# Performance work log

Hardware: AMD Instinct MI355X
Metric: run time of the kernel (lower is better)

The kernel has to match this reference:

```python
import jax, jax.numpy as jnp
import numpy as np

TOKENS, D_IN, D_OUT, RANK = 16384, 4096, 4096, 512

def setup_inputs() -> dict:
    key = jax.random.key(0)
    k1, k2, k3, k4 = jax.random.split(key, 4)
    x = jax.random.normal(k1, (TOKENS, D_IN), dtype=jnp.float32)
    U = jax.random.normal(k2, (D_OUT, RANK), dtype=jnp.float32) * 0.02
    sigma = jax.random.uniform(k3, (RANK,), dtype=jnp.float32)
    V = jax.random.normal(k4, (D_IN, RANK), dtype=jnp.float32) * 0.02
    return {"x": x, "U": U, "sigma": sigma, "V": V}

def reference(x, U, sigma, V):
    # W = U @ diag(sigma) @ V.T  (shape [out, in]); out = x @ W.T
    # diag(sigma) contraction expressed as a column scale of U (same math).
    W = (U * sigma[None, :]) @ V.T          # [out, in]
    return x @ W.T                          # [tokens, out]
```

## Files before the change

kernel.cpp:

```cpp
#include <hip/hip_runtime.h>

typedef __bf16 bf16;
typedef __bf16 bf16x4 __attribute__((ext_vector_type(4)));
typedef __bf16 bf16x8 __attribute__((ext_vector_type(8)));
typedef float  f32x4  __attribute__((ext_vector_type(4)));

#define TOKENS 16384
#define D_IN   4096
#define D_OUT  4096
#define RANK   512

__device__ inline void gload_lds16(const bf16* g, bf16* l) {
    __builtin_amdgcn_global_load_lds((const __attribute__((address_space(1))) void*)g,
                                     (__attribute__((address_space(3))) void*)l,
                                     16, 0, 0);
}

__global__ __launch_bounds__(256) void vt_scale(const float* __restrict__ V,
                                                const float* __restrict__ sg,
                                                bf16* __restrict__ Vst) {
    __shared__ float tile[64][65];
    const int tx = threadIdx.x & 63;
    const int ty = threadIdx.x >> 6;
    const int kb = blockIdx.x * 64;
    const int rb = blockIdx.y * 64;
    const float s = sg[rb + tx];
#pragma unroll
    for (int i = ty; i < 64; i += 4)
        tile[i][tx] = V[(size_t)(kb + i) * RANK + rb + tx] * s;
    __syncthreads();
#pragma unroll
    for (int i = ty; i < 64; i += 4) {
        int r = rb + i;
        int kp = kb + (tx ^ ((r & 7) << 3));
        Vst[(size_t)r * D_IN + kp] = (bf16)tile[tx][i];
    }
}

__global__ __launch_bounds__(256) void cvt_bf16_4(const float* __restrict__ in,
                                                  bf16* __restrict__ o, int n4) {
    int i = blockIdx.x * 256 + threadIdx.x;
    if (i < n4) {
        f32x4 v = *(const f32x4*)(in + (size_t)i * 4);
        bf16x4 b = { (bf16)v[0], (bf16)v[1], (bf16)v[2], (bf16)v[3] };
        *(bf16x4*)(o + (size_t)i * 4) = b;
    }
}

__global__ __launch_bounds__(256) void gemm1_swz(const float* __restrict__ A,
                                                 const bf16* __restrict__ B,
                                                 bf16* __restrict__ T,
                                                 int M, int N, int K) {
    __shared__ bf16 Al[128 * 64];
    __shared__ bf16 Bl[128 * 64];

    const int t  = threadIdx.x;
    const int l  = t & 63;
    const int w  = t >> 6;
    const int wr = w >> 1, wc = w & 1;
    const int lr = l & 15;
    const int kg = l >> 4;
    const int sxor = (lr & 7) << 3;

    const int nwg = gridDim.x;
    const int bid = blockIdx.x;
    const int cpx = nwg >> 3;
    const int swz = (bid & 7) * cpx + (bid >> 3);
    const int ntn = N >> 7;
    const int tm  = (swz / ntn) << 7;
    const int tn  = (swz % ntn) << 7;

    const int arow  = t >> 4;
    const int acg   = t & 15;
    const int awxor = (arow & 7) << 3;
    const float* Ap = A + (size_t)(tm + arow) * K + acg * 4;
    const bf16* Bp  = B + (size_t)(tn + (t >> 3)) * K + (t & 7) * 8;

    f32x4 acc[4][4] = {};

    for (int kt = 0; kt < K; kt += 64) {
#pragma unroll
        for (int c = 0; c < 4; ++c)
            gload_lds16(Bp + kt + (size_t)(c * 32) * K, &Bl[(c * 256 + t) * 8]);
        f32x4 ra[8];
#pragma unroll
        for (int c = 0; c < 8; ++c)
            ra[c] = *(const f32x4*)(Ap + kt + (size_t)(c * 16) * K);
#pragma unroll
        for (int c = 0; c < 8; ++c) {
            bf16x4 b = { (bf16)ra[c][0], (bf16)ra[c][1], (bf16)ra[c][2], (bf16)ra[c][3] };
            *(bf16x4*)&Al[(c * 16 + arow) * 64 + ((acg * 4) ^ awxor)] = b;
        }
        __syncthreads();

#pragma unroll
        for (int ks = 0; ks < 2; ++ks) {
            bf16x8 af[4], bfr[4];
#pragma unroll
            for (int f = 0; f < 4; ++f) {
                af[f]  = *(const bf16x8*)&Al[(wr * 64 + f * 16 + lr) * 64 + ((ks * 32 + kg * 8) ^ sxor)];
                bfr[f] = *(const bf16x8*)&Bl[(wc * 64 + f * 16 + lr) * 64 + ((ks * 32 + kg * 8) ^ sxor)];
            }
#pragma unroll
            for (int fm = 0; fm < 4; ++fm)
#pragma unroll
                for (int fn = 0; fn < 4; ++fn)
                    acc[fm][fn] = __builtin_amdgcn_mfma_f32_16x16x32_bf16(
                        af[fm], bfr[fn], acc[fm][fn], 0, 0, 0);
        }
        __syncthreads();
    }

    const int r0 = tm + wr * 64 + kg * 4;
    const int c0 = tn + wc * 64 + lr;
#pragma unroll
    for (int fm = 0; fm < 4; ++fm)
#pragma unroll
        for (int fn = 0; fn < 4; ++fn)
#pragma unroll
            for (int r = 0; r < 4; ++r)
                T[(size_t)(r0 + fm * 16 + r) * N + (c0 + fn * 16)] = (bf16)acc[fm][fn][r];
}

__global__ __launch_bounds__(256) void gemm2_bt(const bf16* __restrict__ A,
                                                const bf16* __restrict__ B,
                                                float* __restrict__ out,
                                                int M, int N, int K) {
    __shared__ bf16 Al[128 * 64];
    __shared__ bf16 Bl[128 * 64];

    const int t  = threadIdx.x;
    const int l  = t & 63;
    const int w  = t >> 6;
    const int wr = w >> 1, wc = w & 1;
    const int lr = l & 15;
    const int kg = l >> 4;

    const int nwg = gridDim.x;
    const int bid = blockIdx.x;
    const int cpx = nwg >> 3;
    const int swz = (bid & 7) * cpx + (bid >> 3);
    const int ntn = N >> 7;
    const int tm  = (swz / ntn) << 7;
    const int tn  = (swz % ntn) << 7;

    f32x4 acc[4][4] = {};

    for (int kt = 0; kt < K; kt += 64) {
#pragma unroll
        for (int c = 0; c < 4; ++c) {
            int i = c * 256 + t;
            gload_lds16(A + (size_t)(tm + (i >> 3)) * K + kt + (i & 7) * 8, &Al[i * 8]);
        }
#pragma unroll
        for (int c = 0; c < 4; ++c) {
            int i = c * 256 + t;
            gload_lds16(B + (size_t)(tn + (i >> 3)) * K + kt + (i & 7) * 8, &Bl[i * 8]);
        }
        __syncthreads();

#pragma unroll
        for (int ks = 0; ks < 2; ++ks) {
            bf16x8 af[4], bfr[4];
#pragma unroll
            for (int f = 0; f < 4; ++f) {
                af[f]  = *(const bf16x8*)&Al[(wr * 64 + f * 16 + lr) * 64 + ks * 32 + kg * 8];
                bfr[f] = *(const bf16x8*)&Bl[(wc * 64 + f * 16 + lr) * 64 + ks * 32 + kg * 8];
            }
#pragma unroll
            for (int fm = 0; fm < 4; ++fm)
#pragma unroll
                for (int fn = 0; fn < 4; ++fn)
                    acc[fm][fn] = __builtin_amdgcn_mfma_f32_16x16x32_bf16(
                        af[fm], bfr[fn], acc[fm][fn], 0, 0, 0);
        }
        __syncthreads();
    }

    const int r0 = tm + wr * 64 + kg * 4;
    const int c0 = tn + wc * 64 + lr;
#pragma unroll
    for (int fm = 0; fm < 4; ++fm)
#pragma unroll
        for (int fn = 0; fn < 4; ++fn)
#pragma unroll
            for (int r = 0; r < 4; ++r)
                out[(size_t)(r0 + fm * 16 + r) * N + (c0 + fn * 16)] = acc[fm][fn][r];
}

extern "C" void kernel_launch(void* const* d_in, const int* in_sizes, int n_in,
                              void* d_out, int out_size, void* d_ws, size_t ws_size,
                              hipStream_t stream) {
    const float* x  = (const float*)d_in[0];
    const float* U  = (const float*)d_in[1];
    const float* sg = (const float*)d_in[2];
    const float* V  = (const float*)d_in[3];
    float* out = (float*)d_out;

    char* ws = (char*)d_ws;
    bf16* Vst = (bf16*)ws;
    bf16* Ub  = (bf16*)(ws + (4u << 20));
    bf16* T   = (bf16*)(ws + (8u << 20));

    vt_scale<<<dim3(D_IN / 64, RANK / 64), 256, 0, stream>>>(V, sg, Vst);
    cvt_bf16_4<<<(D_OUT * RANK / 4 + 255) / 256, 256, 0, stream>>>(U, Ub, D_OUT * RANK / 4);

    gemm1_swz<<<(TOKENS / 128) * (RANK / 128), 256, 0, stream>>>(
        x, Vst, T, TOKENS, RANK, D_IN);

    gemm2_bt<<<(TOKENS / 128) * (D_OUT / 128), 256, 0, stream>>>(
        T, Ub, out, TOKENS, D_OUT, RANK);
}
```

Before: 268.3 us.

## Split-K the first GEMM into two halves with a separate reduction kernel

The first GEMM (x @ Vs^T) originally launched only 512 workgroups, each looping over the full K=4096. It now launches 1024 workgroups, each handling half of K, and writes fp32 partial sums to a workspace. A new reduce kernel adds the two partials and converts the sum to bf16 T. The intent is more workgroups in flight on the many-CU GPU, at the cost of an extra kernel launch and about 64 MB of extra fp32 traffic for the partials.

```diff
diff --git a/kernel.cpp b/kernel.cpp
--- a/kernel.cpp
+++ b/kernel.cpp
@@ -47,10 +47,10 @@
     }
 }
 
-__global__ __launch_bounds__(256) void gemm1_swz(const float* __restrict__ A,
-                                                 const bf16* __restrict__ B,
-                                                 bf16* __restrict__ T,
-                                                 int M, int N, int K) {
+__global__ __launch_bounds__(256) void gemm1_sk(const float* __restrict__ A,
+                                                const bf16* __restrict__ B,
+                                                float* __restrict__ P,
+                                                int M, int N, int Kfull, int Khalf) {
     __shared__ bf16 Al[128 * 64];
     __shared__ bf16 Bl[128 * 64];
 
@@ -66,26 +66,29 @@
     const int bid = blockIdx.x;
     const int cpx = nwg >> 3;
     const int swz = (bid & 7) * cpx + (bid >> 3);
+    const int khalf  = swz >> 9;
+    const int tileid = swz & 511;
     const int ntn = N >> 7;
-    const int tm  = (swz / ntn) << 7;
-    const int tn  = (swz % ntn) << 7;
+    const int tm  = (tileid / ntn) << 7;
+    const int tn  = (tileid % ntn) << 7;
+    const int kbase = khalf * Khalf;
 
     const int arow  = t >> 4;
     const int acg   = t & 15;
     const int awxor = (arow & 7) << 3;
-    const float* Ap = A + (size_t)(tm + arow) * K + acg * 4;
-    const bf16* Bp  = B + (size_t)(tn + (t >> 3)) * K + (t & 7) * 8;
+    const float* Ap = A + (size_t)(tm + arow) * Kfull + kbase + acg * 4;
+    const bf16* Bp  = B + (size_t)(tn + (t >> 3)) * Kfull + kbase + (t & 7) * 8;
 
     f32x4 acc[4][4] = {};
 
-    for (int kt = 0; kt < K; kt += 64) {
+    for (int kt = 0; kt < Khalf; kt += 64) {
 #pragma unroll
         for (int c = 0; c < 4; ++c)
-            gload_lds16(Bp + kt + (size_t)(c * 32) * K, &Bl[(c * 256 + t) * 8]);
+            gload_lds16(Bp + kt + (size_t)(c * 32) * Kfull, &Bl[(c * 256 + t) * 8]);
         f32x4 ra[8];
 #pragma unroll
         for (int c = 0; c < 8; ++c)
-            ra[c] = *(const f32x4*)(Ap + kt + (size_t)(c * 16) * K);
+            ra[c] = *(const f32x4*)(Ap + kt + (size_t)(c * 16) * Kfull);
 #pragma unroll
         for (int c = 0; c < 8; ++c) {
             bf16x4 b = { (bf16)ra[c][0], (bf16)ra[c][1], (bf16)ra[c][2], (bf16)ra[c][3] };
@@ -111,6 +114,7 @@
         __syncthreads();
     }
 
+    float* Po = P + (size_t)khalf * M * N;
     const int r0 = tm + wr * 64 + kg * 4;
     const int c0 = tn + wc * 64 + lr;
 #pragma unroll
@@ -119,7 +123,20 @@
         for (int fn = 0; fn < 4; ++fn)
 #pragma unroll
             for (int r = 0; r < 4; ++r)
-                T[(size_t)(r0 + fm * 16 + r) * N + (c0 + fn * 16)] = (bf16)acc[fm][fn][r];
+                Po[(size_t)(r0 + fm * 16 + r) * N + (c0 + fn * 16)] = acc[fm][fn][r];
+}
+
+__global__ __launch_bounds__(256) void reduce_T(const float* __restrict__ P,
+                                                bf16* __restrict__ T, int n4) {
+    const float* P1 = P + (size_t)TOKENS * RANK;
+    int stride = gridDim.x * 256;
+    for (int i = blockIdx.x * 256 + threadIdx.x; i < n4; i += stride) {
+        f32x4 a = *(const f32x4*)(P  + (size_t)i * 4);
+        f32x4 b = *(const f32x4*)(P1 + (size_t)i * 4);
+        bf16x4 o = { (bf16)(a[0] + b[0]), (bf16)(a[1] + b[1]),
+                     (bf16)(a[2] + b[2]), (bf16)(a[3] + b[3]) };
+        *(bf16x4*)(T + (size_t)i * 4) = o;
+    }
 }
 
 __global__ __launch_bounds__(256) void gemm2_bt(const bf16* __restrict__ A,
@@ -198,15 +215,18 @@
     float* out = (float*)d_out;
 
     char* ws = (char*)d_ws;
-    bf16* Vst = (bf16*)ws;
-    bf16* Ub  = (bf16*)(ws + (4u << 20));
-    bf16* T   = (bf16*)(ws + (8u << 20));
+    bf16*  Vst = (bf16*)ws;
+    bf16*  Ub  = (bf16*)(ws + (4u << 20));
+    bf16*  T   = (bf16*)(ws + (8u << 20));
+    float* Pf  = (float*)(ws + (32u << 20));
 
     vt_scale<<<dim3(D_IN / 64, RANK / 64), 256, 0, stream>>>(V, sg, Vst);
     cvt_bf16_4<<<(D_OUT * RANK / 4 + 255) / 256, 256, 0, stream>>>(U, Ub, D_OUT * RANK / 4);
 
-    gemm1_swz<<<(TOKENS / 128) * (RANK / 128), 256, 0, stream>>>(
-        x, Vst, T, TOKENS, RANK, D_IN);
+    gemm1_sk<<<2 * (TOKENS / 128) * (RANK / 128), 256, 0, stream>>>(
+        x, Vst, Pf, TOKENS, RANK, D_IN, D_IN / 2);
+
+    reduce_T<<<2048, 256, 0, stream>>>(Pf, T, TOKENS * RANK / 4);
 
     gemm2_bt<<<(TOKENS / 128) * (D_OUT / 128), 256, 0, stream>>>(
         T, Ub, out, TOKENS, D_OUT, RANK);
```

Result: slower. 321.5 us (+19.8%).
